# Kernel tuning notes

Measured on AMD Instinct MI355X. Metric: run time of the kernel, lower is better.

Reference implementation:

```python
import jax, jax.numpy as jnp
import numpy as np

N_NODES = 20000
N_EDGES = 320000
F_IN = 128
H = 4        # heads per layer
D = 128      # per-head hidden dim
NEG_SLOPE = 0.2


def setup_inputs() -> dict:
    key = jax.random.key(0)
    ks = jax.random.split(key, 14)
    s = 0.05
    inp = {
        "feats": jax.random.normal(ks[0], (N_NODES, F_IN), jnp.float32),
        "src": jax.random.randint(ks[1], (N_EDGES,), 0, N_NODES, jnp.int64),
        "dst": jax.random.randint(ks[2], (N_EDGES,), 0, N_NODES, jnp.int64),
        # layer 1: in F_IN -> H heads x D, flatten agg
        "W1": s * jax.random.normal(ks[3], (F_IN, H * D), jnp.float32),
        "al1": s * jax.random.normal(ks[4], (H, D), jnp.float32),
        "ar1": s * jax.random.normal(ks[5], (H, D), jnp.float32),
        "b1": jnp.zeros((H * D,), jnp.float32),
        # layer 2: in H*D -> H heads x D, mean agg
        "W2": s * jax.random.normal(ks[6], (H * D, H * D), jnp.float32),
        "al2": s * jax.random.normal(ks[7], (H, D), jnp.float32),
        "ar2": s * jax.random.normal(ks[8], (H, D), jnp.float32),
        "b2": jnp.zeros((H * D,), jnp.float32),
        # readout Linear(D, 1)
        "Wr": s * jax.random.normal(ks[9], (D, 1), jnp.float32),
        "br": jnp.zeros((1,), jnp.float32),
    }
    return inp


def _gat_conv(x, src, dst, W, al, ar, b, n_nodes):
    """dgl GATConv: per-head linear, edge softmax over incoming edges, scatter-sum."""
    h, d = al.shape
    z = (x @ W).reshape(n_nodes, h, d)                      # [N,H,D]
    el = jnp.einsum('nhd,hd->nh', z, al)                    # [N,H]
    er = jnp.einsum('nhd,hd->nh', z, ar)                    # [N,H]
    e = jax.nn.leaky_relu(el[src] + er[dst], NEG_SLOPE)     # [E,H]
    # numerically stable softmax grouped by destination node
    emax = jax.lax.stop_gradient(jax.ops.segment_max(e, dst, num_segments=n_nodes))
    a = jnp.exp(e - emax[dst])                              # [E,H]
    denom = jax.ops.segment_sum(a, dst, num_segments=n_nodes)
    alpha = a / jnp.maximum(denom[dst], 1e-9)               # [E,H]
    out = jax.ops.segment_sum(alpha[:, :, None] * z[src], dst, num_segments=n_nodes)
    return out + b.reshape(1, h, d)                         # [N,H,D]


def reference(feats, src, dst, W1, al1, ar1, b1, W2, al2, ar2, b2, Wr, br):
    n = feats.shape[0]
    h1 = _gat_conv(feats, src, dst, W1, al1, ar1, b1, n)    # [N,H,D]
    h1 = jax.nn.elu(h1.reshape(n, -1))                      # flatten heads -> [N,H*D]
    h2 = _gat_conv(h1, src, dst, W2, al2, ar2, b2, n)       # [N,H,D]
    h2 = h2.mean(axis=1)                                    # mean over heads -> [N,D]
    node_preds = h2 @ Wr + br                               # [N,1]
    return node_preds.sum(axis=0)                           # [1]
```

## Files before the change

### kernel.cpp

```cpp
#include <hip/hip_runtime.h>
#include <hip/hip_bf16.h>
#include <cstddef>

constexpr int NN = 20000;
constexpr int NE = 320000;
constexpr int NHEAD = 4;
constexpr int HD = 512;
constexpr int MPAD = 20096;
constexpr int SLOTS = 64;
constexpr float NEG_SLOPE = 0.2f;

using short8 = __attribute__((ext_vector_type(8))) short;
using f32x4 = __attribute__((ext_vector_type(4))) float;

__device__ inline void gload16(const void* g, void* l) {
  __builtin_amdgcn_global_load_lds(
      (const __attribute__((address_space(1))) void*)g,
      (__attribute__((address_space(3))) void*)l, 16, 0, 0);
}

__device__ inline float fastrcp(float x) { return __builtin_amdgcn_rcpf(x); }

__device__ inline float fast_elu(float x) {
  return (x > 0.f) ? x : (__expf(x) - 1.0f);
}

constexpr int S0 = NN;
constexpr int S1 = S0 + NN * 128 / 4;
constexpr int S2 = S1 + 512 * 128;
constexpr int S3 = S2 + 4 * 16 * 128;
constexpr int S4 = S3 + 1024;
constexpr int S5 = S4 + 60000;
constexpr int S6 = S5 + 256;
__global__ __launch_bounds__(256) void prep_kernel(
    const float* __restrict__ feats, const float* __restrict__ W1,
    const float* __restrict__ W2, const float* __restrict__ al1,
    const float* __restrict__ ar1, const float* __restrict__ al2,
    const float* __restrict__ ar2, const float* __restrict__ Wr,
    __hip_bfloat16* __restrict__ featsb, __hip_bfloat16* __restrict__ W1t,
    __hip_bfloat16* __restrict__ vcombh, float* __restrict__ wl1t,
    float* __restrict__ wr1t, float* __restrict__ zero3,
    float* __restrict__ partials, int* __restrict__ cnt) {
  int t = blockIdx.x * 256 + threadIdx.x;
  if (t < S0) {
    cnt[t] = 0;
  } else if (t < S1) {
    int u = (t - S0) * 4;
    float4 f = *reinterpret_cast<const float4*>(&feats[u]);
    __hip_bfloat162 o0 = __float22bfloat162_rn(make_float2(f.x, f.y));
    __hip_bfloat162 o1 = __float22bfloat162_rn(make_float2(f.z, f.w));
    uint2 pk;
    pk.x = *reinterpret_cast<unsigned int*>(&o0);
    pk.y = *reinterpret_cast<unsigned int*>(&o1);
    *reinterpret_cast<uint2*>(&featsb[u]) = pk;
  } else if (t < S2) {
    int u = t - S1;
    W1t[u] = __float2bfloat16(W1[(size_t)(u & 127) * 512 + (u >> 7)]);
  } else if (t < S3) {
    int u = t - S2;
    int head = u >> 11, rem = u & 2047;
    int m = rem >> 7, kk = rem & 127;
    float s = 0.f;
    if (m < 12) {
      int h = m & 3;
      const float* vec = (m < 4) ? (al2 + h * 128)
                       : (m < 8) ? (ar2 + h * 128) : Wr;
      const float* wrow = W2 + (size_t)(head * 128 + kk) * 512 + h * 128;
      for (int d = 0; d < 128; ++d) s += wrow[d] * vec[d];
    }
    int slot = kk >> 3, e = kk & 7;
    int sl = slot ^ (m & 7);
    vcombh[head * 2048 + m * 128 + sl * 8 + e] = __float2bfloat16(s);
  } else if (t < S4) {
    int u = t - S3;
    int d = u >> 3, rem = u & 7, h = rem >> 1, sel = rem & 1;
    const float* vec = (sel ? ar1 : al1) + h * 128;
    const float* wrow = W1 + (size_t)d * 512 + h * 128;
    float s = 0.f;
    for (int dd = 0; dd < 128; ++dd) s += wrow[dd] * vec[dd];
    (sel ? wr1t : wl1t)[d * 4 + h] = s;
  } else if (t < S5) {
    int u = (t - S4) * 4;
    *reinterpret_cast<float4*>(&zero3[u]) = make_float4(0.f, 0.f, 0.f, 0.f);
  } else if (t < S6) {
    partials[t - S5] = 0.f;
  }
}

__global__ __launch_bounds__(256) void fill_logits_kernel(
    const int* __restrict__ src, const int* __restrict__ dst,
    int* __restrict__ cnt, int* __restrict__ src_perm,
    const __hip_bfloat16* __restrict__ featsb,
    const float* __restrict__ wl1t, const float* __restrict__ wr1t,
    float* __restrict__ el1, float* __restrict__ er1) {
  int t = threadIdx.x;
  {
    int nth = gridDim.x * 256;
    int gid = blockIdx.x * 256 + t;
    for (int e = gid; e < NE; e += nth) {
      int d = dst[e];
      int p = atomicAdd(&cnt[d], 1);
      if (p < SLOTS) src_perm[d * SLOTS + p] = src[e];
    }
  }
  int wv = t >> 6, lane = t & 63;
  int n = blockIdx.x * 4 + wv;
  unsigned int uu = *reinterpret_cast<const unsigned int*>(
      &featsb[(size_t)n * 128 + 2 * lane]);
  __hip_bfloat162 ub = *reinterpret_cast<__hip_bfloat162*>(&uu);
  float2 f = __bfloat1622float2(ub);
  float4 wlA = *reinterpret_cast<const float4*>(&wl1t[lane * 8]);
  float4 wlB = *reinterpret_cast<const float4*>(&wl1t[lane * 8 + 4]);
  float4 wrA = *reinterpret_cast<const float4*>(&wr1t[lane * 8]);
  float4 wrB = *reinterpret_cast<const float4*>(&wr1t[lane * 8 + 4]);
  float p0 = f.x * wlA.x + f.y * wlB.x;
  float p1 = f.x * wlA.y + f.y * wlB.y;
  float p2 = f.x * wlA.z + f.y * wlB.z;
  float p3 = f.x * wlA.w + f.y * wlB.w;
  float p4 = f.x * wrA.x + f.y * wrB.x;
  float p5 = f.x * wrA.y + f.y * wrB.y;
  float p6 = f.x * wrA.z + f.y * wrB.z;
  float p7 = f.x * wrA.w + f.y * wrB.w;
#pragma unroll
  for (int off = 1; off < 64; off <<= 1) {
    p0 += __shfl_xor(p0, off); p1 += __shfl_xor(p1, off);
    p2 += __shfl_xor(p2, off); p3 += __shfl_xor(p3, off);
    p4 += __shfl_xor(p4, off); p5 += __shfl_xor(p5, off);
    p6 += __shfl_xor(p6, off); p7 += __shfl_xor(p7, off);
  }
  if (lane == 0) {
    *reinterpret_cast<float4*>(&el1[n * 4]) = make_float4(p0, p1, p2, p3);
    *reinterpret_cast<float4*>(&er1[n * 4]) = make_float4(p4, p5, p6, p7);
  }
}

__global__ __launch_bounds__(256) void gather_kernel(
    const __hip_bfloat16* __restrict__ featsb,
    const int* __restrict__ cnt, const int* __restrict__ src_perm,
    const float* __restrict__ el, const float* __restrict__ er,
    __hip_bfloat16* __restrict__ aggb) {
  __shared__ float4 alph[4][SLOTS];
  __shared__ int srcb[4][SLOTS];
  int wv = __builtin_amdgcn_readfirstlane((int)(threadIdx.x >> 6));
  int n = blockIdx.x * 4 + wv;
  int lane = threadIdx.x & 63;
  int c = min(cnt[n], SLOTS);

  {
    float4 er4 = *reinterpret_cast<const float4*>(&er[n * 4]);
    float a0 = 0.f, a1 = 0.f, a2 = 0.f, a3 = 0.f;
    int sv = 0;
    if (lane < c) {
      sv = src_perm[n * SLOTS + lane];
      float4 e4 = *reinterpret_cast<const float4*>(&el[sv * 4]);
      float x0 = e4.x + er4.x, x1 = e4.y + er4.y;
      float x2 = e4.z + er4.z, x3 = e4.w + er4.w;
      x0 = (x0 > 0.f) ? x0 : NEG_SLOPE * x0;
      x1 = (x1 > 0.f) ? x1 : NEG_SLOPE * x1;
      x2 = (x2 > 0.f) ? x2 : NEG_SLOPE * x2;
      x3 = (x3 > 0.f) ? x3 : NEG_SLOPE * x3;
      a0 = __expf(x0); a1 = __expf(x1); a2 = __expf(x2); a3 = __expf(x3);
    }
    float s0 = a0, s1 = a1, s2 = a2, s3 = a3;
#pragma unroll
    for (int off = 1; off < 64; off <<= 1) {
      s0 += __shfl_xor(s0, off);
      s1 += __shfl_xor(s1, off);
      s2 += __shfl_xor(s2, off);
      s3 += __shfl_xor(s3, off);
    }
    float i0 = fastrcp(fmaxf(s0, 1e-9f));
    float i1 = fastrcp(fmaxf(s1, 1e-9f));
    float i2 = fastrcp(fmaxf(s2, 1e-9f));
    float i3 = fastrcp(fmaxf(s3, 1e-9f));
    alph[wv][lane] = make_float4(a0 * i0, a1 * i1, a2 * i2, a3 * i3);
    srcb[wv][lane] = sv;
  }

  float acc[4][2] = {};

#define EB(IDX)                                                                \
  {                                                                            \
    float4 a4 = alph[wv][(IDX)];                                               \
    int s = srcb[wv][(IDX)];                                                   \
    unsigned int uu = *reinterpret_cast<const unsigned int*>(                  \
        &featsb[(size_t)s * 128 + 2 * lane]);                                  \
    __hip_bfloat162 ub = *reinterpret_cast<__hip_bfloat162*>(&uu);             \
    float2 f = __bfloat1622float2(ub);                                         \
    acc[0][0] += a4.x * f.x; acc[0][1] += a4.x * f.y;                          \
    acc[1][0] += a4.y * f.x; acc[1][1] += a4.y * f.y;                          \
    acc[2][0] += a4.z * f.x; acc[2][1] += a4.z * f.y;                          \
    acc[3][0] += a4.w * f.x; acc[3][1] += a4.w * f.y;                          \
  }

  int i = 0;
  for (; i + 3 < c; i += 4) {
    EB(i) EB(i + 1) EB(i + 2) EB(i + 3)
  }
  for (; i < c; ++i) EB(i)
#undef EB

  size_t obase = (size_t)n * HD + 2 * lane;
#pragma unroll
  for (int h = 0; h < 4; ++h) {
    __hip_bfloat162 o = __float22bfloat162_rn(make_float2(acc[h][0], acc[h][1]));
    *reinterpret_cast<unsigned int*>(&aggb[obase + h * 128]) =
        *reinterpret_cast<unsigned int*>(&o);
  }
}

__global__ __launch_bounds__(256) void h1_gemm_kernel(
    const __hip_bfloat16* __restrict__ A,
    const __hip_bfloat16* __restrict__ Bt,
    const __hip_bfloat16* __restrict__ vcombh,
    const float* __restrict__ b1,
    float* __restrict__ elq,
    float* __restrict__ er2) {
  __shared__ short AsH[64 * 128];
  __shared__ short Bs[128 * 128];
  __shared__ short Vc[16 * 128];
  int t = threadIdx.x;
  int lane = t & 63, wave = t >> 6;
  int rowBase = blockIdx.x * 64;
  int head = blockIdx.y;
  int nloc = lane & 15;
  int quad = lane >> 4;

#pragma unroll
  for (int p = 0; p < 4; ++p) {
    int fbase = p * 256 + wave * 64;
    int f = fbase + lane;
    int row = f >> 4, slot = f & 15;
    int ss = slot ^ (row & 7);
    gload16(A + (size_t)(rowBase + row) * HD + head * 128 + ss * 8,
            AsH + fbase * 8);
  }
#pragma unroll
  for (int p = 0; p < 8; ++p) {
    int fbase = p * 256 + wave * 64;
    int f = fbase + lane;
    int row = f >> 4, slot = f & 15;
    int ss = slot ^ (row & 7);
    gload16(Bt + (size_t)(head * 128 + row) * 128 + ss * 8,
            Bs + fbase * 8);
  }
  {
    int fbase = wave * 64;
    gload16(vcombh + head * 2048 + (size_t)(fbase + lane) * 8,
            Vc + fbase * 8);
  }
  __syncthreads();

  f32x4 acc[8];
#pragma unroll
  for (int i = 0; i < 8; ++i) acc[i] = (f32x4){0.f, 0.f, 0.f, 0.f};
#pragma unroll
  for (int c = 0; c < 4; ++c) {
    int arow = wave * 16 + nloc;
    short8 bfr = *(const short8*)&AsH[arow * 128 +
                                      (((c << 2) + quad) ^ (arow & 7)) * 8];
#pragma unroll
    for (int i = 0; i < 8; ++i) {
      int brow = i * 16 + nloc;
      short8 af = *(const short8*)&Bs[brow * 128 +
                                      (((c << 2) + quad) ^ (brow & 7)) * 8];
      acc[i] = __builtin_amdgcn_mfma_f32_16x16x32_bf16(af, bfr, acc[i], 0, 0, 0);
    }
  }

  int node = wave * 16 + nloc;
#pragma unroll
  for (int i = 0; i < 8; ++i) {
    float4 b4 = *reinterpret_cast<const float4*>(
        &b1[head * 128 + i * 16 + quad * 4]);
    float e0 = fast_elu(acc[i][0] + b4.x);
    float e1 = fast_elu(acc[i][1] + b4.y);
    float e2 = fast_elu(acc[i][2] + b4.z);
    float e3 = fast_elu(acc[i][3] + b4.w);
    __hip_bfloat162 p0 = __float22bfloat162_rn(make_float2(e0, e1));
    __hip_bfloat162 p1 = __float22bfloat162_rn(make_float2(e2, e3));
    uint2 pk;
    pk.x = *reinterpret_cast<unsigned int*>(&p0);
    pk.y = *reinterpret_cast<unsigned int*>(&p1);
    int slot = i * 2 + (quad >> 1);
    int sub = quad & 1;
    int sl = slot ^ (node & 7);
    *reinterpret_cast<uint2*>(&AsH[node * 128 + sl * 8 + sub * 4]) = pk;
  }

  f32x4 acc2 = (f32x4){0.f, 0.f, 0.f, 0.f};
#pragma unroll
  for (int c = 0; c < 4; ++c) {
    short8 a2 = *(const short8*)&Vc[nloc * 128 +
                                    (((c << 2) + quad) ^ (nloc & 7)) * 8];
    short8 b2 = *(const short8*)&AsH[node * 128 +
                                     (((c << 2) + quad) ^ (node & 7)) * 8];
    acc2 = __builtin_amdgcn_mfma_f32_16x16x32_bf16(a2, b2, acc2, 0, 0, 0);
  }

  int gn = rowBase + node;
  if (gn < NN) {
    if (quad == 0) {
#pragma unroll
      for (int r = 0; r < 4; ++r)
        atomicAdd(&elq[(size_t)gn * 8 + r], acc2[r]);
    } else if (quad == 1) {
#pragma unroll
      for (int r = 0; r < 4; ++r)
        atomicAdd(&er2[(size_t)gn * 4 + r], acc2[r]);
    } else if (quad == 2) {
#pragma unroll
      for (int r = 0; r < 4; ++r)
        atomicAdd(&elq[(size_t)gn * 8 + 4 + r], acc2[r]);
    }
  }
}

__global__ __launch_bounds__(256) void attn_q_kernel(
    const int* __restrict__ src_perm,
    const int* __restrict__ cnt,
    const float* __restrict__ elq,
    const float* __restrict__ er2,
    float* __restrict__ partials) {
  __shared__ float blk[4];
  int wv = __builtin_amdgcn_readfirstlane((int)(threadIdx.x >> 6));
  int n = blockIdx.x * 4 + wv;
  int lane = threadIdx.x & 63;
  int c = min(cnt[n], SLOTS);
  float4 er4 = *reinterpret_cast<const float4*>(&er2[n * 4]);
  float a0 = 0.f, a1 = 0.f, a2 = 0.f, a3 = 0.f;
  float4 q4 = make_float4(0.f, 0.f, 0.f, 0.f);
  if (lane < c) {
    int s = src_perm[n * SLOTS + lane];
    float4 e4 = *reinterpret_cast<const float4*>(&elq[(size_t)s * 8]);
    q4 = *reinterpret_cast<const float4*>(&elq[(size_t)s * 8 + 4]);
    float x0 = e4.x + er4.x, x1 = e4.y + er4.y;
    float x2 = e4.z + er4.z, x3 = e4.w + er4.w;
    x0 = (x0 > 0.f) ? x0 : NEG_SLOPE * x0;
    x1 = (x1 > 0.f) ? x1 : NEG_SLOPE * x1;
    x2 = (x2 > 0.f) ? x2 : NEG_SLOPE * x2;
    x3 = (x3 > 0.f) ? x3 : NEG_SLOPE * x3;
    a0 = __expf(x0); a1 = __expf(x1); a2 = __expf(x2); a3 = __expf(x3);
  }
  float s0 = a0, s1 = a1, s2 = a2, s3 = a3;
#pragma unroll
  for (int off = 1; off < 64; off <<= 1) {
    s0 += __shfl_xor(s0, off);
    s1 += __shfl_xor(s1, off);
    s2 += __shfl_xor(s2, off);
    s3 += __shfl_xor(s3, off);
  }
  float p = 0.f;
  if (lane < c) {
    p = (a0 * fastrcp(fmaxf(s0, 1e-9f))) * q4.x +
        (a1 * fastrcp(fmaxf(s1, 1e-9f))) * q4.y +
        (a2 * fastrcp(fmaxf(s2, 1e-9f))) * q4.z +
        (a3 * fastrcp(fmaxf(s3, 1e-9f))) * q4.w;
  }
#pragma unroll
  for (int off = 32; off > 0; off >>= 1) p += __shfl_down(p, off);
  if (lane == 0) blk[wv] = p;
  __syncthreads();
  if (threadIdx.x == 0) {
    atomicAdd(&partials[blockIdx.x & 255], blk[0] + blk[1] + blk[2] + blk[3]);
  }
}

__global__ __launch_bounds__(512) void final_kernel(
    const float* __restrict__ partials, const float* __restrict__ b2,
    const float* __restrict__ Wr, const float* __restrict__ br,
    float* __restrict__ out) {
  __shared__ float tmp[512];
  int t = threadIdx.x;
  float sum = (t < 256) ? partials[t] : 0.f;
  sum += (float)NN * b2[t] * Wr[t & 127];
  tmp[t] = sum;
  __syncthreads();
  for (int off = 256; off > 0; off >>= 1) {
    if (t < off) tmp[t] += tmp[t + off];
    __syncthreads();
  }
  if (t == 0) out[0] = 0.25f * tmp[0] + (float)NN * br[0];
}

extern "C" void kernel_launch(void* const* d_in, const int* in_sizes, int n_in,
                              void* d_out, int out_size, void* d_ws, size_t ws_size,
                              hipStream_t stream) {
  const float* feats = (const float*)d_in[0];
  const int* src = (const int*)d_in[1];
  const int* dst = (const int*)d_in[2];
  const float* W1 = (const float*)d_in[3];
  const float* al1 = (const float*)d_in[4];
  const float* ar1 = (const float*)d_in[5];
  const float* b1 = (const float*)d_in[6];
  const float* W2 = (const float*)d_in[7];
  const float* al2 = (const float*)d_in[8];
  const float* ar2 = (const float*)d_in[9];
  const float* b2 = (const float*)d_in[10];
  const float* Wr = (const float*)d_in[11];
  const float* br = (const float*)d_in[12];
  float* out = (float*)d_out;

  __hip_bfloat16* featsb = (__hip_bfloat16*)d_ws;
  __hip_bfloat16* aggb = featsb + (size_t)NN * 128;
  __hip_bfloat16* W1t = aggb + (size_t)MPAD * HD;
  __hip_bfloat16* vcombh = W1t + 512 * 128;
  float* wl1t = (float*)(vcombh + 4 * 16 * 128);
  float* wr1t = wl1t + 512;
  float* el1 = wr1t + 512;
  float* er1 = el1 + (size_t)NN * NHEAD;
  float* elq = er1 + (size_t)NN * NHEAD;
  float* er2 = elq + (size_t)NN * 8;
  float* partials = er2 + (size_t)NN * NHEAD;
  int* cnt = (int*)(partials + 256);
  int* src_perm = cnt + NN;

  prep_kernel<<<(S6 + 255) / 256, 256, 0, stream>>>(
      feats, W1, W2, al1, ar1, al2, ar2, Wr, featsb, W1t, vcombh, wl1t, wr1t,
      elq, partials, cnt);

  fill_logits_kernel<<<NN / 4, 256, 0, stream>>>(
      src, dst, cnt, src_perm, featsb, wl1t, wr1t, el1, er1);

  gather_kernel<<<NN / 4, 256, 0, stream>>>(featsb, cnt, src_perm, el1, er1,
                                            aggb);

  dim3 h1grid(MPAD / 64, NHEAD);
  h1_gemm_kernel<<<h1grid, 256, 0, stream>>>(aggb, W1t, vcombh, b1, elq, er2);

  attn_q_kernel<<<NN / 4, 256, 0, stream>>>(src_perm, cnt, elq, er2, partials);
  final_kernel<<<1, 512, 0, stream>>>(partials, b2, Wr, br, out);
}
```

Baseline: 170.9 us.

## Fuse all stages into one persistent cooperative kernel with grid syncs

Replaces the six separate kernel launches with a single persistent cooperative kernel that runs prep, edge bucketing plus logits, gather, the layer-1 GEMM, attention and the final reduction as phases separated by grid.sync. The goal is to remove per-launch overhead and the inter-kernel gaps. In the GEMM phase each block stages its B/V weights once and loops over tiles. The original multi-kernel path is kept as a fallback. The trade-off is a grid capped at 1024 blocks, so each phase loses parallelism and the grid barriers add their own cost. The head-per-block mapping (bid&3) also relies on gridX being a multiple of 4.

Result: slower. 396.9 us (+132.2%).

```diff
diff --git a/kernel.cpp b/kernel.cpp
--- a/kernel.cpp
+++ b/kernel.cpp
@@ -1,12 +1,16 @@
 #include <hip/hip_runtime.h>
+#include <hip/hip_cooperative_groups.h>
 #include <hip/hip_bf16.h>
 #include <cstddef>
+
+namespace cg = cooperative_groups;
 
 constexpr int NN = 20000;
 constexpr int NE = 320000;
 constexpr int NHEAD = 4;
 constexpr int HD = 512;
 constexpr int MPAD = 20096;
+constexpr int NT = (MPAD / 64) * NHEAD;
 constexpr int SLOTS = 64;
 constexpr float NEG_SLOPE = 0.2f;
 
@@ -32,16 +36,13 @@
 constexpr int S4 = S3 + 1024;
 constexpr int S5 = S4 + 60000;
 constexpr int S6 = S5 + 256;
-__global__ __launch_bounds__(256) void prep_kernel(
-    const float* __restrict__ feats, const float* __restrict__ W1,
-    const float* __restrict__ W2, const float* __restrict__ al1,
-    const float* __restrict__ ar1, const float* __restrict__ al2,
-    const float* __restrict__ ar2, const float* __restrict__ Wr,
-    __hip_bfloat16* __restrict__ featsb, __hip_bfloat16* __restrict__ W1t,
-    __hip_bfloat16* __restrict__ vcombh, float* __restrict__ wl1t,
-    float* __restrict__ wr1t, float* __restrict__ zero3,
-    float* __restrict__ partials, int* __restrict__ cnt) {
-  int t = blockIdx.x * 256 + threadIdx.x;
+
+__device__ __forceinline__ void dev_prep_item(
+    int t, const float* feats, const float* W1, const float* W2,
+    const float* al1, const float* ar1, const float* al2, const float* ar2,
+    const float* Wr, __hip_bfloat16* featsb, __hip_bfloat16* W1t,
+    __hip_bfloat16* vcombh, float* wl1t, float* wr1t, float* zero3,
+    float* partials, int* cnt) {
   if (t < S0) {
     cnt[t] = 0;
   } else if (t < S1) {
@@ -87,24 +88,16 @@
   }
 }
 
-__global__ __launch_bounds__(256) void fill_logits_kernel(
-    const int* __restrict__ src, const int* __restrict__ dst,
-    int* __restrict__ cnt, int* __restrict__ src_perm,
-    const __hip_bfloat16* __restrict__ featsb,
-    const float* __restrict__ wl1t, const float* __restrict__ wr1t,
-    float* __restrict__ el1, float* __restrict__ er1) {
-  int t = threadIdx.x;
-  {
-    int nth = gridDim.x * 256;
-    int gid = blockIdx.x * 256 + t;
-    for (int e = gid; e < NE; e += nth) {
-      int d = dst[e];
-      int p = atomicAdd(&cnt[d], 1);
-      if (p < SLOTS) src_perm[d * SLOTS + p] = src[e];
-    }
-  }
-  int wv = t >> 6, lane = t & 63;
-  int n = blockIdx.x * 4 + wv;
+__device__ __forceinline__ void dev_fill_edge(
+    int e, const int* src, const int* dst, int* cnt, int* src_perm) {
+  int d = dst[e];
+  int p = atomicAdd(&cnt[d], 1);
+  if (p < SLOTS) src_perm[d * SLOTS + p] = src[e];
+}
+
+__device__ __forceinline__ void dev_logits_node(
+    int n, int lane, const __hip_bfloat16* featsb, const float* wl1t,
+    const float* wr1t, float* el1, float* er1) {
   unsigned int uu = *reinterpret_cast<const unsigned int*>(
       &featsb[(size_t)n * 128 + 2 * lane]);
   __hip_bfloat162 ub = *reinterpret_cast<__hip_bfloat162*>(&uu);
@@ -134,18 +127,11 @@
   }
 }
 
-__global__ __launch_bounds__(256) void gather_kernel(
-    const __hip_bfloat16* __restrict__ featsb,
-    const int* __restrict__ cnt, const int* __restrict__ src_perm,
-    const float* __restrict__ el, const float* __restrict__ er,
-    __hip_bfloat16* __restrict__ aggb) {
-  __shared__ float4 alph[4][SLOTS];
-  __shared__ int srcb[4][SLOTS];
-  int wv = __builtin_amdgcn_readfirstlane((int)(threadIdx.x >> 6));
-  int n = blockIdx.x * 4 + wv;
-  int lane = threadIdx.x & 63;
+__device__ __forceinline__ void dev_gather_node(
+    int n, int lane, float4* alphW, int* srcbW,
+    const __hip_bfloat16* featsb, const int* cnt, const int* src_perm,
+    const float* el, const float* er, __hip_bfloat16* aggb) {
   int c = min(cnt[n], SLOTS);
-
   {
     float4 er4 = *reinterpret_cast<const float4*>(&er[n * 4]);
     float a0 = 0.f, a1 = 0.f, a2 = 0.f, a3 = 0.f;
@@ -173,16 +159,15 @@
     float i1 = fastrcp(fmaxf(s1, 1e-9f));
     float i2 = fastrcp(fmaxf(s2, 1e-9f));
     float i3 = fastrcp(fmaxf(s3, 1e-9f));
-    alph[wv][lane] = make_float4(a0 * i0, a1 * i1, a2 * i2, a3 * i3);
-    srcb[wv][lane] = sv;
+    alphW[lane] = make_float4(a0 * i0, a1 * i1, a2 * i2, a3 * i3);
+    srcbW[lane] = sv;
   }
 
   float acc[4][2] = {};
-
 #define EB(IDX)                                                                \
   {                                                                            \
-    float4 a4 = alph[wv][(IDX)];                                               \
-    int s = srcb[wv][(IDX)];                                                   \
+    float4 a4 = alphW[(IDX)];                                                  \
+    int s = srcbW[(IDX)];                                                      \
     unsigned int uu = *reinterpret_cast<const unsigned int*>(                  \
         &featsb[(size_t)s * 128 + 2 * lane]);                                  \
     __hip_bfloat162 ub = *reinterpret_cast<__hip_bfloat162*>(&uu);             \
@@ -192,11 +177,8 @@
     acc[2][0] += a4.z * f.x; acc[2][1] += a4.z * f.y;                          \
     acc[3][0] += a4.w * f.x; acc[3][1] += a4.w * f.y;                          \
   }
-
   int i = 0;
-  for (; i + 3 < c; i += 4) {
-    EB(i) EB(i + 1) EB(i + 2) EB(i + 3)
-  }
+  for (; i + 3 < c; i += 4) { EB(i) EB(i + 1) EB(i + 2) EB(i + 3) }
   for (; i < c; ++i) EB(i)
 #undef EB
 
@@ -209,23 +191,26 @@
   }
 }
 
-__global__ __launch_bounds__(256) void h1_gemm_kernel(
-    const __hip_bfloat16* __restrict__ A,
-    const __hip_bfloat16* __restrict__ Bt,
-    const __hip_bfloat16* __restrict__ vcombh,
-    const float* __restrict__ b1,
-    float* __restrict__ elq,
-    float* __restrict__ er2) {
-  __shared__ short AsH[64 * 128];
-  __shared__ short Bs[128 * 128];
-  __shared__ short Vc[16 * 128];
-  int t = threadIdx.x;
-  int lane = t & 63, wave = t >> 6;
-  int rowBase = blockIdx.x * 64;
-  int head = blockIdx.y;
-  int nloc = lane & 15;
-  int quad = lane >> 4;
-
+__device__ __forceinline__ void dev_stage_BV(
+    int head, int lane, int wave, short* Bs, short* Vc,
+    const __hip_bfloat16* Bt, const __hip_bfloat16* vcombh) {
+#pragma unroll
+  for (int p = 0; p < 8; ++p) {
+    int fbase = p * 256 + wave * 64;
+    int f = fbase + lane;
+    int row = f >> 4, slot = f & 15;
+    int ss = slot ^ (row & 7);
+    gload16(Bt + (size_t)(head * 128 + row) * 128 + ss * 8, Bs + fbase * 8);
+  }
+  {
+    int fbase = wave * 64;
+    gload16(vcombh + head * 2048 + (size_t)(fbase + lane) * 8, Vc + fbase * 8);
+  }
+}
+
+__device__ __forceinline__ void dev_stage_A(
+    int rowBase, int head, int lane, int wave, short* AsH,
+    const __hip_bfloat16* A) {
 #pragma unroll
   for (int p = 0; p < 4; ++p) {
     int fbase = p * 256 + wave * 64;
@@ -235,21 +220,12 @@
     gload16(A + (size_t)(rowBase + row) * HD + head * 128 + ss * 8,
             AsH + fbase * 8);
   }
-#pragma unroll
-  for (int p = 0; p < 8; ++p) {
-    int fbase = p * 256 + wave * 64;
-    int f = fbase + lane;
-    int row = f >> 4, slot = f & 15;
-    int ss = slot ^ (row & 7);
-    gload16(Bt + (size_t)(head * 128 + row) * 128 + ss * 8,
-            Bs + fbase * 8);
-  }
-  {
-    int fbase = wave * 64;
-    gload16(vcombh + head * 2048 + (size_t)(fbase + lane) * 8,
-            Vc + fbase * 8);
-  }
-  __syncthreads();
+}
+
+__device__ __forceinline__ void dev_h1_compute(
+    int rowBase, int head, int lane, int wave, short* AsH, const short* Bs,
+    const short* Vc, const float* b1, float* elq, float* er2) {
+  int nloc = lane & 15, quad = lane >> 4;
 
   f32x4 acc[8];
 #pragma unroll
@@ -293,9 +269,9 @@
   for (int c = 0; c < 4; ++c) {
     short8 a2 = *(const short8*)&Vc[nloc * 128 +
                                     (((c << 2) + quad) ^ (nloc & 7)) * 8];
-    short8 b2 = *(const short8*)&AsH[node * 128 +
-                                     (((c << 2) + quad) ^ (node & 7)) * 8];
-    acc2 = __builtin_amdgcn_mfma_f32_16x16x32_bf16(a2, b2, acc2, 0, 0, 0);
+    short8 b2v = *(const short8*)&AsH[node * 128 +
+                                      (((c << 2) + quad) ^ (node & 7)) * 8];
+    acc2 = __builtin_amdgcn_mfma_f32_16x16x32_bf16(a2, b2v, acc2, 0, 0, 0);
   }
 
   int gn = rowBase + node;
@@ -316,16 +292,9 @@
   }
 }
 
-__global__ __launch_bounds__(256) void attn_q_kernel(
-    const int* __restrict__ src_perm,
-    const int* __restrict__ cnt,
-    const float* __restrict__ elq,
-    const float* __restrict__ er2,
-    float* __restrict__ partials) {
-  __shared__ float blk[4];
-  int wv = __builtin_amdgcn_readfirstlane((int)(threadIdx.x >> 6));
-  int n = blockIdx.x * 4 + wv;
-  int lane = threadIdx.x & 63;
+__device__ __forceinline__ float dev_attn_node(
+    int n, int lane, const int* src_perm, const int* cnt,
+    const float* elq, const float* er2) {
   int c = min(cnt[n], SLOTS);
   float4 er4 = *reinterpret_cast<const float4*>(&er2[n * 4]);
   float a0 = 0.f, a1 = 0.f, a2 = 0.f, a3 = 0.f;
@@ -359,11 +328,173 @@
   }
 #pragma unroll
   for (int off = 32; off > 0; off >>= 1) p += __shfl_down(p, off);
+  return p;
+}
+
+struct MegaSmem {
+  short AsH[64 * 128];
+  short Bs[128 * 128];
+  short Vc[16 * 128];
+  float4 alph[4][SLOTS];
+  int srcb[4][SLOTS];
+  float blk[4];
+};
+
+__global__ __launch_bounds__(256, 2) void mega_kernel(
+    const float* __restrict__ feats, const float* __restrict__ W1,
+    const float* __restrict__ W2, const float* __restrict__ al1,
+    const float* __restrict__ ar1, const float* __restrict__ al2,
+    const float* __restrict__ ar2, const float* __restrict__ Wr,
+    const float* __restrict__ b1, const float* __restrict__ b2,
+    const float* __restrict__ br, const int* __restrict__ src,
+    const int* __restrict__ dst, __hip_bfloat16* __restrict__ featsb,
+    __hip_bfloat16* __restrict__ W1t, __hip_bfloat16* __restrict__ vcombh,
+    float* __restrict__ wl1t, float* __restrict__ wr1t,
+    float* __restrict__ el1, float* __restrict__ er1,
+    __hip_bfloat16* __restrict__ aggb, float* __restrict__ elq,
+    float* __restrict__ er2, float* __restrict__ partials,
+    int* __restrict__ cnt, int* __restrict__ src_perm,
+    float* __restrict__ out) {
+  cg::grid_group grid = cg::this_grid();
+  __shared__ MegaSmem sm;
+  const int t = threadIdx.x;
+  const int lane = t & 63, wv = t >> 6;
+  const int bid = blockIdx.x, nb = gridDim.x;
+  const int gtid = bid * 256 + t, nthr = nb * 256;
+  const int gwave = bid * 4 + wv, nwaves = nb * 4;
+
+  for (int u = gtid; u < S6; u += nthr)
+    dev_prep_item(u, feats, W1, W2, al1, ar1, al2, ar2, Wr, featsb, W1t,
+                  vcombh, wl1t, wr1t, elq, partials, cnt);
+  grid.sync();
+
+  for (int e = gtid; e < NE; e += nthr)
+    dev_fill_edge(e, src, dst, cnt, src_perm);
+  for (int n = gwave; n < NN; n += nwaves)
+    dev_logits_node(n, lane, featsb, wl1t, wr1t, el1, er1);
+  grid.sync();
+
+  {
+    float4* alphW = &sm.alph[wv][0];
+    int* srcbW = &sm.srcb[wv][0];
+    for (int n = gwave; n < NN; n += nwaves)
+      dev_gather_node(n, lane, alphW, srcbW, featsb, cnt, src_perm, el1, er1,
+                      aggb);
+  }
+  grid.sync();
+
+  {
+    int head = bid & 3;
+    dev_stage_BV(head, lane, wv, sm.Bs, sm.Vc, W1t, vcombh);
+    for (int tile = bid; tile < NT; tile += nb) {
+      int rowBase = (tile >> 2) * 64;
+      __syncthreads();
+      dev_stage_A(rowBase, head, lane, wv, sm.AsH, aggb);
+      __syncthreads();
+      dev_h1_compute(rowBase, head, lane, wv, sm.AsH, sm.Bs, sm.Vc, b1, elq,
+                     er2);
+    }
+  }
+  grid.sync();
+
+  {
+    float wsum = 0.f;
+    for (int n = gwave; n < NN; n += nwaves)
+      wsum += dev_attn_node(n, lane, src_perm, cnt, elq, er2);
+    if (lane == 0) sm.blk[wv] = wsum;
+    __syncthreads();
+    if (t == 0)
+      atomicAdd(&partials[bid & 255],
+                sm.blk[0] + sm.blk[1] + sm.blk[2] + sm.blk[3]);
+  }
+  grid.sync();
+
+  if (bid == 0) {
+    float* tmp = reinterpret_cast<float*>(&sm.alph[0][0]);
+    float sum = partials[t] +
+                (float)NN * Wr[t & 127] * (b2[t] + b2[t + 256]);
+    tmp[t] = sum;
+    __syncthreads();
+    for (int off = 128; off > 0; off >>= 1) {
+      if (t < off) tmp[t] += tmp[t + off];
+      __syncthreads();
+    }
+    if (t == 0) out[0] = 0.25f * tmp[0] + (float)NN * br[0];
+  }
+}
+
+__global__ __launch_bounds__(256) void prep_kernel(
+    const float* __restrict__ feats, const float* __restrict__ W1,
+    const float* __restrict__ W2, const float* __restrict__ al1,
+    const float* __restrict__ ar1, const float* __restrict__ al2,
+    const float* __restrict__ ar2, const float* __restrict__ Wr,
+    __hip_bfloat16* __restrict__ featsb, __hip_bfloat16* __restrict__ W1t,
+    __hip_bfloat16* __restrict__ vcombh, float* __restrict__ wl1t,
+    float* __restrict__ wr1t, float* __restrict__ zero3,
+    float* __restrict__ partials, int* __restrict__ cnt) {
+  int t = blockIdx.x * 256 + threadIdx.x;
+  dev_prep_item(t, feats, W1, W2, al1, ar1, al2, ar2, Wr, featsb, W1t, vcombh,
+                wl1t, wr1t, zero3, partials, cnt);
+}
+
+__global__ __launch_bounds__(256) void fill_logits_kernel(
+    const int* __restrict__ src, const int* __restrict__ dst,
+    int* __restrict__ cnt, int* __restrict__ src_perm,
+    const __hip_bfloat16* __restrict__ featsb,
+    const float* __restrict__ wl1t, const float* __restrict__ wr1t,
+    float* __restrict__ el1, float* __restrict__ er1) {
+  int t = threadIdx.x;
+  int nth = gridDim.x * 256;
+  int gid = blockIdx.x * 256 + t;
+  for (int e = gid; e < NE; e += nth) dev_fill_edge(e, src, dst, cnt, src_perm);
+  int wv = t >> 6, lane = t & 63;
+  int n = blockIdx.x * 4 + wv;
+  dev_logits_node(n, lane, featsb, wl1t, wr1t, el1, er1);
+}
+
+__global__ __launch_bounds__(256) void gather_kernel(
+    const __hip_bfloat16* __restrict__ featsb, const int* __restrict__ cnt,
+    const int* __restrict__ src_perm, const float* __restrict__ el,
+    const float* __restrict__ er, __hip_bfloat16* __restrict__ aggb) {
+  __shared__ float4 alph[4][SLOTS];
+  __shared__ int srcb[4][SLOTS];
+  int wv = __builtin_amdgcn_readfirstlane((int)(threadIdx.x >> 6));
+  int n = blockIdx.x * 4 + wv;
+  int lane = threadIdx.x & 63;
+  dev_gather_node(n, lane, &alph[wv][0], &srcb[wv][0], featsb, cnt, src_perm,
+                  el, er, aggb);
+}
+
+__global__ __launch_bounds__(256) void h1_gemm_kernel(
+    const __hip_bfloat16* __restrict__ A, const __hip_bfloat16* __restrict__ Bt,
+    const __hip_bfloat16* __restrict__ vcombh, const float* __restrict__ b1,
+    float* __restrict__ elq, float* __restrict__ er2) {
+  __shared__ short AsH[64 * 128];
+  __shared__ short Bs[128 * 128];
+  __shared__ short Vc[16 * 128];
+  int t = threadIdx.x;
+  int lane = t & 63, wave = t >> 6;
+  int rowBase = blockIdx.x * 64;
+  int head = blockIdx.y;
+  dev_stage_A(rowBase, head, lane, wave, AsH, A);
+  dev_stage_BV(head, lane, wave, Bs, Vc, Bt, vcombh);
+  __syncthreads();
+  dev_h1_compute(rowBase, head, lane, wave, AsH, Bs, Vc, b1, elq, er2);
+}
+
+__global__ __launch_bounds__(256) void attn_q_kernel(
+    const int* __restrict__ src_perm, const int* __restrict__ cnt,
+    const float* __restrict__ elq, const float* __restrict__ er2,
+    float* __restrict__ partials) {
+  __shared__ float blk[4];
+  int wv = __builtin_amdgcn_readfirstlane((int)(threadIdx.x >> 6));
+  int n = blockIdx.x * 4 + wv;
+  int lane = threadIdx.x & 63;
+  float p = dev_attn_node(n, lane, src_perm, cnt, elq, er2);
   if (lane == 0) blk[wv] = p;
   __syncthreads();
-  if (threadIdx.x == 0) {
+  if (threadIdx.x == 0)
     atomicAdd(&partials[blockIdx.x & 255], blk[0] + blk[1] + blk[2] + blk[3]);
-  }
 }
 
 __global__ __launch_bounds__(512) void final_kernel(
@@ -415,19 +546,47 @@
   int* cnt = (int*)(partials + 256);
   int* src_perm = cnt + NN;
 
-  prep_kernel<<<(S6 + 255) / 256, 256, 0, stream>>>(
-      feats, W1, W2, al1, ar1, al2, ar2, Wr, featsb, W1t, vcombh, wl1t, wr1t,
-      elq, partials, cnt);
-
-  fill_logits_kernel<<<NN / 4, 256, 0, stream>>>(
-      src, dst, cnt, src_perm, featsb, wl1t, wr1t, el1, er1);
-
-  gather_kernel<<<NN / 4, 256, 0, stream>>>(featsb, cnt, src_perm, el1, er1,
-                                            aggb);
-
-  dim3 h1grid(MPAD / 64, NHEAD);
-  h1_gemm_kernel<<<h1grid, 256, 0, stream>>>(aggb, W1t, vcombh, b1, elq, er2);
-
-  attn_q_kernel<<<NN / 4, 256, 0, stream>>>(src_perm, cnt, elq, er2, partials);
-  final_kernel<<<1, 512, 0, stream>>>(partials, b2, Wr, br, out);
-}
+  static int gridX = -1;
+  if (gridX < 0) {
+    int nbPerCU = 0;
+    hipError_t qe = hipOccupancyMaxActiveBlocksPerMultiprocessor(
+        &nbPerCU, (const void*)mega_kernel, 256, 0);
+    if (qe != hipSuccess || nbPerCU < 1) nbPerCU = 0;
+    int g = nbPerCU * 256;
+    if (g > 1024) g = 1024;
+    g &= ~3;
+    gridX = (g >= 4) ? g : 0;
+  }
+
+  bool coop_ok = false;
+  if (gridX > 0) {
+    void* args[] = {
+        (void*)&feats, (void*)&W1,  (void*)&W2,  (void*)&al1, (void*)&ar1,
+        (void*)&al2,   (void*)&ar2, (void*)&Wr,  (void*)&b1,  (void*)&b2,
+        (void*)&br,    (void*)&src, (void*)&dst, (void*)&featsb,
+        (void*)&W1t,   (void*)&vcombh, (void*)&wl1t, (void*)&wr1t,
+        (void*)&el1,   (void*)&er1, (void*)&aggb, (void*)&elq, (void*)&er2,
+        (void*)&partials, (void*)&cnt, (void*)&src_perm, (void*)&out};
+    hipError_t le = hipLaunchCooperativeKernel(
+        reinterpret_cast<void*>(mega_kernel), dim3(gridX), dim3(256), args, 0,
+        stream);
+    coop_ok = (le == hipSuccess);
+    if (!coop_ok) gridX = 0;
+  }
+
+  if (!coop_ok) {
+    prep_kernel<<<(S6 + 255) / 256, 256, 0, stream>>>(
+        feats, W1, W2, al1, ar1, al2, ar2, Wr, featsb, W1t, vcombh, wl1t,
+        wr1t, elq, partials, cnt);
+    fill_logits_kernel<<<NN / 4, 256, 0, stream>>>(
+        src, dst, cnt, src_perm, featsb, wl1t, wr1t, el1, er1);
+    gather_kernel<<<NN / 4, 256, 0, stream>>>(featsb, cnt, src_perm, el1, er1,
+                                              aggb);
+    dim3 h1grid(MPAD / 64, NHEAD);
+    h1_gemm_kernel<<<h1grid, 256, 0, stream>>>(aggb, W1t, vcombh, b1, elq,
+                                               er2);
+    attn_q_kernel<<<NN / 4, 256, 0, stream>>>(src_perm, cnt, elq, er2,
+                                              partials);
+    final_kernel<<<1, 512, 0, stream>>>(partials, b2, Wr, br, out);
+  }
+}
```

## Widen per-lane loads in logits/gather and reuse GEMM weight tile across two row blocks

Applied to the files above, without the earlier changes.

The logits kernel now gives each node to a 32-lane half-wave with 8-byte loads, so each block handles 8 nodes and the grid is halved. The gather kernel has each half-wave process alternate edges with 8-byte feature loads, then combines the halves with a cross-lane shuffle. The h1 GEMM loads the W1t and Vc tiles once per block and loops over two 64-row A tiles, halving the grid and the redundant weight loads. The cost is fewer blocks for latency hiding, an extra barrier inside the GEMM loop, and odd edge counts in gather leaning on zero-padded alpha slots.

Result: no change. 173.9 us (+1.8%).

```diff
diff --git a/kernel.cpp b/kernel.cpp
--- a/kernel.cpp
+++ b/kernel.cpp
@@ -104,33 +104,38 @@
     }
   }
   int wv = t >> 6, lane = t & 63;
-  int n = blockIdx.x * 4 + wv;
-  unsigned int uu = *reinterpret_cast<const unsigned int*>(
-      &featsb[(size_t)n * 128 + 2 * lane]);
-  __hip_bfloat162 ub = *reinterpret_cast<__hip_bfloat162*>(&uu);
-  float2 f = __bfloat1622float2(ub);
-  float4 wlA = *reinterpret_cast<const float4*>(&wl1t[lane * 8]);
-  float4 wlB = *reinterpret_cast<const float4*>(&wl1t[lane * 8 + 4]);
-  float4 wrA = *reinterpret_cast<const float4*>(&wr1t[lane * 8]);
-  float4 wrB = *reinterpret_cast<const float4*>(&wr1t[lane * 8 + 4]);
-  float p0 = f.x * wlA.x + f.y * wlB.x;
-  float p1 = f.x * wlA.y + f.y * wlB.y;
-  float p2 = f.x * wlA.z + f.y * wlB.z;
-  float p3 = f.x * wlA.w + f.y * wlB.w;
-  float p4 = f.x * wrA.x + f.y * wrB.x;
-  float p5 = f.x * wrA.y + f.y * wrB.y;
-  float p6 = f.x * wrA.z + f.y * wrB.z;
-  float p7 = f.x * wrA.w + f.y * wrB.w;
-#pragma unroll
-  for (int off = 1; off < 64; off <<= 1) {
-    p0 += __shfl_xor(p0, off); p1 += __shfl_xor(p1, off);
-    p2 += __shfl_xor(p2, off); p3 += __shfl_xor(p3, off);
-    p4 += __shfl_xor(p4, off); p5 += __shfl_xor(p5, off);
-    p6 += __shfl_xor(p6, off); p7 += __shfl_xor(p7, off);
-  }
-  if (lane == 0) {
-    *reinterpret_cast<float4*>(&el1[n * 4]) = make_float4(p0, p1, p2, p3);
-    *reinterpret_cast<float4*>(&er1[n * 4]) = make_float4(p4, p5, p6, p7);
+  int half = lane >> 5, l5 = lane & 31;
+  int n = blockIdx.x * 8 + wv * 2 + half;
+  int d0 = l5 * 4;
+  uint2 w = *reinterpret_cast<const uint2*>(&featsb[(size_t)n * 128 + d0]);
+  __hip_bfloat162 u0 = *reinterpret_cast<__hip_bfloat162*>(&w.x);
+  __hip_bfloat162 u1 = *reinterpret_cast<__hip_bfloat162*>(&w.y);
+  float2 fA = __bfloat1622float2(u0);
+  float2 fB = __bfloat1622float2(u1);
+  float f[4] = {fA.x, fA.y, fB.x, fB.y};
+  float pl[4] = {0.f, 0.f, 0.f, 0.f}, pr[4] = {0.f, 0.f, 0.f, 0.f};
+#pragma unroll
+  for (int j = 0; j < 4; ++j) {
+    float4 wl = *reinterpret_cast<const float4*>(&wl1t[(d0 + j) * 4]);
+    float4 wr = *reinterpret_cast<const float4*>(&wr1t[(d0 + j) * 4]);
+    pl[0] += f[j] * wl.x; pl[1] += f[j] * wl.y;
+    pl[2] += f[j] * wl.z; pl[3] += f[j] * wl.w;
+    pr[0] += f[j] * wr.x; pr[1] += f[j] * wr.y;
+    pr[2] += f[j] * wr.z; pr[3] += f[j] * wr.w;
+  }
+#pragma unroll
+  for (int off = 1; off < 32; off <<= 1) {
+#pragma unroll
+    for (int k = 0; k < 4; ++k) {
+      pl[k] += __shfl_xor(pl[k], off);
+      pr[k] += __shfl_xor(pr[k], off);
+    }
+  }
+  if (l5 == 0) {
+    *reinterpret_cast<float4*>(&el1[n * 4]) =
+        make_float4(pl[0], pl[1], pl[2], pl[3]);
+    *reinterpret_cast<float4*>(&er1[n * 4]) =
+        make_float4(pr[0], pr[1], pr[2], pr[3]);
   }
 }
 
@@ -177,35 +182,49 @@
     srcb[wv][lane] = sv;
   }
 
-  float acc[4][2] = {};
-
-#define EB(IDX)                                                                \
+  int half = lane >> 5, l5 = lane & 31;
+  int d0 = l5 * 4;
+  float acc[4][4] = {};
+
+#define PR(I)                                                                  \
   {                                                                            \
-    float4 a4 = alph[wv][(IDX)];                                               \
-    int s = srcb[wv][(IDX)];                                                   \
-    unsigned int uu = *reinterpret_cast<const unsigned int*>(                  \
-        &featsb[(size_t)s * 128 + 2 * lane]);                                  \
-    __hip_bfloat162 ub = *reinterpret_cast<__hip_bfloat162*>(&uu);             \
-    float2 f = __bfloat1622float2(ub);                                         \
-    acc[0][0] += a4.x * f.x; acc[0][1] += a4.x * f.y;                          \
-    acc[1][0] += a4.y * f.x; acc[1][1] += a4.y * f.y;                          \
-    acc[2][0] += a4.z * f.x; acc[2][1] += a4.z * f.y;                          \
-    acc[3][0] += a4.w * f.x; acc[3][1] += a4.w * f.y;                          \
+    int e = (I) + half;                                                        \
+    float4 a4 = alph[wv][e];                                                   \
+    int s = srcb[wv][e];                                                       \
+    uint2 w = *reinterpret_cast<const uint2*>(&featsb[(size_t)s * 128 + d0]);  \
+    __hip_bfloat162 u0 = *reinterpret_cast<__hip_bfloat162*>(&w.x);            \
+    __hip_bfloat162 u1 = *reinterpret_cast<__hip_bfloat162*>(&w.y);            \
+    float2 fA = __bfloat1622float2(u0);                                        \
+    float2 fB = __bfloat1622float2(u1);                                        \
+    acc[0][0] += a4.x * fA.x; acc[0][1] += a4.x * fA.y;                        \
+    acc[0][2] += a4.x * fB.x; acc[0][3] += a4.x * fB.y;                        \
+    acc[1][0] += a4.y * fA.x; acc[1][1] += a4.y * fA.y;                        \
+    acc[1][2] += a4.y * fB.x; acc[1][3] += a4.y * fB.y;                        \
+    acc[2][0] += a4.z * fA.x; acc[2][1] += a4.z * fA.y;                        \
+    acc[2][2] += a4.z * fB.x; acc[2][3] += a4.z * fB.y;                        \
+    acc[3][0] += a4.w * fA.x; acc[3][1] += a4.w * fA.y;                        \
+    acc[3][2] += a4.w * fB.x; acc[3][3] += a4.w * fB.y;                        \
   }
 
   int i = 0;
-  for (; i + 3 < c; i += 4) {
-    EB(i) EB(i + 1) EB(i + 2) EB(i + 3)
-  }
-  for (; i < c; ++i) EB(i)
-#undef EB
-
-  size_t obase = (size_t)n * HD + 2 * lane;
-#pragma unroll
-  for (int h = 0; h < 4; ++h) {
-    __hip_bfloat162 o = __float22bfloat162_rn(make_float2(acc[h][0], acc[h][1]));
-    *reinterpret_cast<unsigned int*>(&aggb[obase + h * 128]) =
-        *reinterpret_cast<unsigned int*>(&o);
+  for (; i + 3 < c; i += 4) { PR(i) PR(i + 2) }
+  for (; i < c; i += 2) PR(i)
+#undef PR
+
+#pragma unroll
+  for (int h = 0; h < 4; ++h)
+#pragma unroll
+    for (int j = 0; j < 4; ++j) acc[h][j] += __shfl_xor(acc[h][j], 32);
+
+#pragma unroll
+  for (int hh = 0; hh < 2; ++hh) {
+    int h = half * 2 + hh;
+    __hip_bfloat162 o0 = __float22bfloat162_rn(make_float2(acc[h][0], acc[h][1]));
+    __hip_bfloat162 o1 = __float22bfloat162_rn(make_float2(acc[h][2], acc[h][3]));
+    uint2 pk;
+    pk.x = *reinterpret_cast<unsigned int*>(&o0);
+    pk.y = *reinterpret_cast<unsigned int*>(&o1);
+    *reinterpret_cast<uint2*>(&aggb[(size_t)n * HD + h * 128 + d0]) = pk;
   }
 }
 
@@ -221,97 +240,100 @@
   __shared__ short Vc[16 * 128];
   int t = threadIdx.x;
   int lane = t & 63, wave = t >> 6;
-  int rowBase = blockIdx.x * 64;
   int head = blockIdx.y;
-  int nloc = lane & 15;
-  int quad = lane >> 4;
-
-#pragma unroll
-  for (int p = 0; p < 4; ++p) {
-    int fbase = p * 256 + wave * 64;
-    int f = fbase + lane;
-    int row = f >> 4, slot = f & 15;
-    int ss = slot ^ (row & 7);
-    gload16(A + (size_t)(rowBase + row) * HD + head * 128 + ss * 8,
-            AsH + fbase * 8);
-  }
+  int nloc = lane & 15, quad = lane >> 4;
+
 #pragma unroll
   for (int p = 0; p < 8; ++p) {
     int fbase = p * 256 + wave * 64;
     int f = fbase + lane;
     int row = f >> 4, slot = f & 15;
     int ss = slot ^ (row & 7);
-    gload16(Bt + (size_t)(head * 128 + row) * 128 + ss * 8,
-            Bs + fbase * 8);
+    gload16(Bt + (size_t)(head * 128 + row) * 128 + ss * 8, Bs + fbase * 8);
   }
   {
     int fbase = wave * 64;
-    gload16(vcombh + head * 2048 + (size_t)(fbase + lane) * 8,
-            Vc + fbase * 8);
-  }
-  __syncthreads();
-
-  f32x4 acc[8];
-#pragma unroll
-  for (int i = 0; i < 8; ++i) acc[i] = (f32x4){0.f, 0.f, 0.f, 0.f};
-#pragma unroll
-  for (int c = 0; c < 4; ++c) {
-    int arow = wave * 16 + nloc;
-    short8 bfr = *(const short8*)&AsH[arow * 128 +
-                                      (((c << 2) + quad) ^ (arow & 7)) * 8];
+    gload16(vcombh + head * 2048 + (size_t)(fbase + lane) * 8, Vc + fbase * 8);
+  }
+
+  for (int it = 0; it < 2; ++it) {
+    int rowBase = (blockIdx.x * 2 + it) * 64;
+    if (it) __syncthreads();
+
+#pragma unroll
+    for (int p = 0; p < 4; ++p) {
+      int fbase = p * 256 + wave * 64;
+      int f = fbase + lane;
+      int row = f >> 4, slot = f & 15;
+      int ss = slot ^ (row & 7);
+      gload16(A + (size_t)(rowBase + row) * HD + head * 128 + ss * 8,
+              AsH + fbase * 8);
+    }
+    __syncthreads();
+
+    f32x4 acc[8];
+#pragma unroll
+    for (int i = 0; i < 8; ++i) acc[i] = (f32x4){0.f, 0.f, 0.f, 0.f};
+#pragma unroll
+    for (int c = 0; c < 4; ++c) {
+      int arow = wave * 16 + nloc;
+      short8 bfr = *(const short8*)&AsH[arow * 128 +
+                                        (((c << 2) + quad) ^ (arow & 7)) * 8];
+#pragma unroll
+      for (int i = 0; i < 8; ++i) {
+        int brow = i * 16 + nloc;
+        short8 af = *(const short8*)&Bs[brow * 128 +
+                                        (((c << 2) + quad) ^ (brow & 7)) * 8];
+        acc[i] = __builtin_amdgcn_mfma_f32_16x16x32_bf16(af, bfr, acc[i],
+                                                         0, 0, 0);
+      }
+    }
+
+    int node = wave * 16 + nloc;
 #pragma unroll
     for (int i = 0; i < 8; ++i) {
-      int brow = i * 16 + nloc;
-      short8 af = *(const short8*)&Bs[brow * 128 +
-                                      (((c << 2) + quad) ^ (brow & 7)) * 8];
-      acc[i] = __builtin_amdgcn_mfma_f32_16x16x32_bf16(af, bfr, acc[i], 0, 0, 0);
-    }
-  }
-
-  int node = wave * 16 + nloc;
-#pragma unroll
-  for (int i = 0; i < 8; ++i) {
-    float4 b4 = *reinterpret_cast<const float4*>(
-        &b1[head * 128 + i * 16 + quad * 4]);
-    float e0 = fast_elu(acc[i][0] + b4.x);
-    float e1 = fast_elu(acc[i][1] + b4.y);
-    float e2 = fast_elu(acc[i][2] + b4.z);
-    float e3 = fast_elu(acc[i][3] + b4.w);
-    __hip_bfloat162 p0 = __float22bfloat162_rn(make_float2(e0, e1));
-    __hip_bfloat162 p1 = __float22bfloat162_rn(make_float2(e2, e3));
-    uint2 pk;
-    pk.x = *reinterpret_cast<unsigned int*>(&p0);
-    pk.y = *reinterpret_cast<unsigned int*>(&p1);
-    int slot = i * 2 + (quad >> 1);
-    int sub = quad & 1;
-    int sl = slot ^ (node & 7);
-    *reinterpret_cast<uint2*>(&AsH[node * 128 + sl * 8 + sub * 4]) = pk;
-  }
-
-  f32x4 acc2 = (f32x4){0.f, 0.f, 0.f, 0.f};
-#pragma unroll
-  for (int c = 0; c < 4; ++c) {
-    short8 a2 = *(const short8*)&Vc[nloc * 128 +
-                                    (((c << 2) + quad) ^ (nloc & 7)) * 8];
-    short8 b2 = *(const short8*)&AsH[node * 128 +
-                                     (((c << 2) + quad) ^ (node & 7)) * 8];
-    acc2 = __builtin_amdgcn_mfma_f32_16x16x32_bf16(a2, b2, acc2, 0, 0, 0);
-  }
-
-  int gn = rowBase + node;
-  if (gn < NN) {
-    if (quad == 0) {
-#pragma unroll
-      for (int r = 0; r < 4; ++r)
-        atomicAdd(&elq[(size_t)gn * 8 + r], acc2[r]);
-    } else if (quad == 1) {
-#pragma unroll
-      for (int r = 0; r < 4; ++r)
-        atomicAdd(&er2[(size_t)gn * 4 + r], acc2[r]);
-    } else if (quad == 2) {
-#pragma unroll
-      for (int r = 0; r < 4; ++r)
-        atomicAdd(&elq[(size_t)gn * 8 + 4 + r], acc2[r]);
+      float4 b4 = *reinterpret_cast<const float4*>(
+          &b1[head * 128 + i * 16 + quad * 4]);
+      float e0 = fast_elu(acc[i][0] + b4.x);
+      float e1 = fast_elu(acc[i][1] + b4.y);
+      float e2 = fast_elu(acc[i][2] + b4.z);
+      float e3 = fast_elu(acc[i][3] + b4.w);
+      __hip_bfloat162 p0 = __float22bfloat162_rn(make_float2(e0, e1));
+      __hip_bfloat162 p1 = __float22bfloat162_rn(make_float2(e2, e3));
+      uint2 pk;
+      pk.x = *reinterpret_cast<unsigned int*>(&p0);
+      pk.y = *reinterpret_cast<unsigned int*>(&p1);
+      int slot = i * 2 + (quad >> 1);
+      int sub = quad & 1;
+      int sl = slot ^ (node & 7);
+      *reinterpret_cast<uint2*>(&AsH[node * 128 + sl * 8 + sub * 4]) = pk;
+    }
+
+    f32x4 acc2 = (f32x4){0.f, 0.f, 0.f, 0.f};
+#pragma unroll
+    for (int c = 0; c < 4; ++c) {
+      short8 a2 = *(const short8*)&Vc[nloc * 128 +
+                                      (((c << 2) + quad) ^ (nloc & 7)) * 8];
+      short8 b2v = *(const short8*)&AsH[node * 128 +
+                                        (((c << 2) + quad) ^ (node & 7)) * 8];
+      acc2 = __builtin_amdgcn_mfma_f32_16x16x32_bf16(a2, b2v, acc2, 0, 0, 0);
+    }
+
+    int gn = rowBase + node;
+    if (gn < NN) {
+      if (quad == 0) {
+#pragma unroll
+        for (int r = 0; r < 4; ++r)
+          atomicAdd(&elq[(size_t)gn * 8 + r], acc2[r]);
+      } else if (quad == 1) {
+#pragma unroll
+        for (int r = 0; r < 4; ++r)
+          atomicAdd(&er2[(size_t)gn * 4 + r], acc2[r]);
+      } else if (quad == 2) {
+#pragma unroll
+        for (int r = 0; r < 4; ++r)
+          atomicAdd(&elq[(size_t)gn * 8 + 4 + r], acc2[r]);
+      }
     }
   }
 }
@@ -419,13 +441,13 @@
       feats, W1, W2, al1, ar1, al2, ar2, Wr, featsb, W1t, vcombh, wl1t, wr1t,
       elq, partials, cnt);
 
-  fill_logits_kernel<<<NN / 4, 256, 0, stream>>>(
+  fill_logits_kernel<<<NN / 8, 256, 0, stream>>>(
       src, dst, cnt, src_perm, featsb, wl1t, wr1t, el1, er1);
 
   gather_kernel<<<NN / 4, 256, 0, stream>>>(featsb, cnt, src_perm, el1, er1,
                                             aggb);
 
-  dim3 h1grid(MPAD / 64, NHEAD);
+  dim3 h1grid(MPAD / 128, NHEAD);
   h1_gemm_kernel<<<h1grid, 256, 0, stream>>>(aggb, W1t, vcombh, b1, elq, er2);
 
   attn_q_kernel<<<NN / 4, 256, 0, stream>>>(src_perm, cnt, elq, er2, partials);
```
